# Kernel tuning notes

Hardware: AMD Instinct MI355X
Metric: run time of the kernel (lower is better)

Reference implementation:

```python
import jax, jax.numpy as jnp
import numpy as np

DEPTH = 256
SEQ = 394
EMB = 300


def _branch(x_nch, W, b, n):
    # W: [depth, n*EMB], flatten order of paragraph[i:i+n,:].flatten() is (time, emb)
    k = W.reshape(DEPTH, n, EMB).transpose(0, 2, 1)  # OIH: [depth, EMB, n]
    y = jax.lax.conv_general_dilated(
        x_nch, k, window_strides=(1,), padding='VALID',
        dimension_numbers=('NCH', 'OIH', 'NCH'))  # [B, depth, SEQ-n+1]
    # original loop only covers windows i = 0 .. SEQ-n-1 (SEQ-n windows)
    y = y[:, :, :SEQ - n] + b  # b: [depth, 1] broadcasts over time
    # running max starts at 0 and relu clamps >= 0; outer relu is a no-op
    return jnp.max(jax.nn.relu(y), axis=-1)  # [B, depth]


def setup_inputs() -> dict:
    key = jax.random.key(0)
    ks = jax.random.split(key, 7)
    inp = {
        'input': jax.random.normal(ks[0], (64, SEQ, EMB), dtype=jnp.float32),
        'W1': jax.random.normal(ks[1], (DEPTH, 3 * EMB), dtype=jnp.float32),
        'W2': jax.random.normal(ks[2], (DEPTH, 4 * EMB), dtype=jnp.float32),
        'W3': jax.random.normal(ks[3], (DEPTH, 5 * EMB), dtype=jnp.float32),
        'b1': jax.random.normal(ks[4], (DEPTH, 1), dtype=jnp.float32),
        'b2': jax.random.normal(ks[5], (DEPTH, 1), dtype=jnp.float32),
        'b3': jax.random.normal(ks[6], (DEPTH, 1), dtype=jnp.float32),
    }
    return inp


def reference(input, W1, W2, W3, b1, b2, b3):
    x = input.transpose(0, 2, 1)  # [B, EMB, SEQ] (NCH)
    o1 = _branch(x, W1, b1, 3)
    o2 = _branch(x, W2, b2, 4)
    o3 = _branch(x, W3, b3, 5)
    return jnp.concatenate([o1, o2, o3], axis=1)  # [B, 3*depth]
```

## Files before the change

kernel.cpp:

```cpp
#include <hip/hip_runtime.h>
#include <hip/hip_bf16.h>

#define SEQ 394
#define EMB 300
#define EMBP 312
#define NROWS (64 * SEQ)
#define XPTOT ((long)NROWS * EMBP)
#define NCHT 118
#define CBE0 29
#define CBE1 68
#define XE 36864
#define WGRAN ((long)NCHT * 1024)

typedef __attribute__((ext_vector_type(8))) short short8;
typedef __attribute__((ext_vector_type(4))) float f32x4;

__device__ __forceinline__ unsigned short f2b(float f) {
    unsigned u = __float_as_uint(f);
    u += 0x7FFFu + ((u >> 16) & 1u);
    return (unsigned short)(u >> 16);
}

__device__ __forceinline__ void gload_lds16(const void* g, void* l) {
    __builtin_amdgcn_global_load_lds(
        (const __attribute__((address_space(1))) void*)g,
        (__attribute__((address_space(3))) void*)l, 16, 0, 0);
}


__global__ __launch_bounds__(256)
void pack_x_kernel(const float* __restrict__ x, unsigned short* __restrict__ xp)
{
    long q = (long)blockIdx.x * 256 + threadIdx.x;
    int row = (int)(q / 78);
    int c4  = ((int)(q - (long)row * 78)) * 4;
    ushort4 u;
    if (c4 < 300) {
        float4 v = *(const float4*)(x + (long)row * 300 + c4);
        u = make_ushort4(f2b(v.x), f2b(v.y), f2b(v.z), f2b(v.w));
    } else {
        u = make_ushort4(0, 0, 0, 0);
    }
    *(ushort4*)(xp + q * 4) = u;
}

__global__ __launch_bounds__(256)
void pack_w_kernel(const float* __restrict__ W1, const float* __restrict__ W2,
                   const float* __restrict__ W3, unsigned short* __restrict__ wb)
{
    int G = blockIdx.x * 256 + threadIdx.x;
    int c    = G >> 10;
    int rem  = G & 1023;
    int fg   = rem >> 7;
    int floc = (rem >> 2) & 31;
    int gs   = rem & 3;
    const float* Wg; int n, cb;
    if (c <= CBE0)      { Wg = W1; n = 3; cb = 0;        }
    else if (c <= CBE1) { Wg = W2; n = 4; cb = CBE0 + 1; }
    else                { Wg = W3; n = 5; cb = CBE1 + 1; }
    const int K = n * 300;
    const int f = fg * 32 + floc;
    const int kl = (c - cb) * 32 + (gs ^ ((floc >> 1) & 3)) * 8;
    unsigned short v[8];
#pragma unroll
    for (int j = 0; j < 8; ++j) {
        int kk = kl + j;
        int r  = kk / EMBP;
        int e  = kk - r * EMBP;
        v[j] = (r < n && e < 300) ? f2b(Wg[(long)f * K + r * 300 + e]) : (unsigned short)0;
    }
    unsigned short* dst = wb + (long)G * 8;
    *(ushort4*)dst       = make_ushort4(v[0], v[1], v[2], v[3]);
    *(ushort4*)(dst + 4) = make_ushort4(v[4], v[5], v[6], v[7]);
}


__global__ __launch_bounds__(512, 2)
void convgemm_kernel(const unsigned short* __restrict__ xp,
                     const unsigned short* __restrict__ wb,
                     const float* __restrict__ b1, const float* __restrict__ b2,
                     const float* __restrict__ b3,
                     float* __restrict__ out)
{
    __shared__ unsigned short LDS[XE + 8 * 4096];

    const int tid  = threadIdx.x;
    const int lane = tid & 63;
    const int wid  = tid >> 6;
    const int lr   = lane & 15, lg = lane >> 4;
    const int b    = blockIdx.x >> 2;
    const int i0   = (blockIdx.x & 3) * 98;

    auto stageW = [&](int cc) {
        const unsigned short* ws = wb + ((long)(cc * 8 + wid)) * 1024 + lane * 8;
        unsigned short* wd = &LDS[XE + wid * 4096 + (cc & 3) * 1024];
        gload_lds16(ws, wd);
        gload_lds16(ws + 512, wd + 512);
    };

    {
        const long xbase = ((long)b * SEQ + i0) * EMBP;
        const long slim  = XPTOT - 8;
#pragma unroll
        for (int rd = 0; rd < 9; ++rd) {
            int g = rd * 512 + wid * 64;
            long se = xbase + (long)(g + lane) * 8;
            if (se > slim) se = slim;
            gload_lds16(xp + se, &LDS[g * 8]);
        }
    }
    stageW(0); stageW(1); stageW(2);
    asm volatile("s_waitcnt vmcnt(0)" ::: "memory");
    __builtin_amdgcn_sched_barrier(0);
    __builtin_amdgcn_s_barrier();
    __builtin_amdgcn_sched_barrier(0);

    f32x4 acc[2][7];
#pragma unroll
    for (int i = 0; i < 2; ++i)
#pragma unroll
        for (int j = 0; j < 7; ++j)
            acc[i][j] = (f32x4)0.0f;

    const int swz = (lg ^ ((lr >> 1) & 3)) * 8;

    auto readFrags = [&](int cc, short8 af[2], short8 bx[7]) {
        const int c0  = (cc <= CBE0) ? 0 : (cc <= CBE1) ? (CBE0 + 1) : (CBE1 + 1);
        const int bxe = (cc - c0) * 32;
        const unsigned short* Wc = &LDS[XE + wid * 4096 + (cc & 3) * 1024];
        af[0] = *(const short8*)&Wc[lr * 32 + swz];
        af[1] = *(const short8*)&Wc[(16 + lr) * 32 + swz];
#pragma unroll
        for (int ni = 0; ni < 7; ++ni)
            bx[ni] = *(const short8*)&LDS[(ni * 16 + lr) * EMBP + bxe + lg * 8];
    };

    auto doMFMA = [&](short8 af[2], short8 bx[7]) {
#pragma unroll
        for (int mi = 0; mi < 2; ++mi)
#pragma unroll
            for (int ni = 0; ni < 7; ++ni)
                acc[mi][ni] = __builtin_amdgcn_mfma_f32_16x16x32_bf16(af[mi], bx[ni], acc[mi][ni], 0, 0, 0);
    };

    auto epilogue = [&](int br) {
        const float* bg = (br == 0) ? b1 : (br == 1) ? b2 : b3;
        const int Nw = 391 - br;
        int wlim = Nw - i0; if (wlim > 112) wlim = 112;
        const int ob = b * 768 + br * 256;
#pragma unroll
        for (int mi = 0; mi < 2; ++mi) {
#pragma unroll
            for (int r = 0; r < 4; ++r) {
                const int d = wid * 32 + mi * 16 + lg * 4 + r;
                const float bv = bg[d];
                float m = 0.f;
#pragma unroll
                for (int ni = 0; ni < 7; ++ni) {
                    int w = ni * 16 + lr;
                    float v = fmaxf(acc[mi][ni][r] + bv, 0.f);
                    if (w >= wlim) v = 0.f;
                    m = fmaxf(m, v);
                }
#pragma unroll
                for (int off = 1; off < 16; off <<= 1)
                    m = fmaxf(m, __shfl_xor(m, off));
                if (lr == 0)
                    atomicMax((int*)(out + ob + d), __float_as_int(m));
            }
        }
#pragma unroll
        for (int i = 0; i < 2; ++i)
#pragma unroll
            for (int j = 0; j < 7; ++j)
                acc[i][j] = (f32x4)0.0f;
    };

    short8 fa0[2], fb0[7], fa1[2], fb1[7];
    readFrags(0, fa0, fb0);

    for (int c = 0; c < NCHT; c += 2) {
        if (c + 3 < NCHT) stageW(c + 3);
        if (c + 3 < NCHT)      asm volatile("s_waitcnt vmcnt(4)" ::: "memory");
        else if (c + 2 < NCHT) asm volatile("s_waitcnt vmcnt(2)" ::: "memory");
        else                   asm volatile("s_waitcnt vmcnt(0)" ::: "memory");
        __builtin_amdgcn_sched_barrier(0);
        readFrags(c + 1, fa1, fb1);
        doMFMA(fa0, fb0);
        if (c == CBE1) epilogue(1);

        const int cc = c + 1;
        if (cc + 3 < NCHT) stageW(cc + 3);
        if (cc + 3 < NCHT)      asm volatile("s_waitcnt vmcnt(4)" ::: "memory");
        else if (cc + 2 < NCHT) asm volatile("s_waitcnt vmcnt(2)" ::: "memory");
        else                    asm volatile("s_waitcnt vmcnt(0)" ::: "memory");
        __builtin_amdgcn_sched_barrier(0);
        if (cc + 1 < NCHT) readFrags(cc + 1, fa0, fb0);
        doMFMA(fa1, fb1);
        if (cc == CBE0) epilogue(0);
        if (cc == NCHT - 1) epilogue(2);
    }
}


__device__ __forceinline__ void load_chunk(const float* __restrict__ Wg,
                                           const float* __restrict__ xb,
                                           int K, int dbase, int i0, int k0, int tid,
                                           float4 wv[4], float4 xv[4])
{
#pragma unroll
    for (int i = 0; i < 4; ++i) {
        int fi  = tid + (i << 8);
        int row = fi >> 3;
        int c4  = (fi & 7) << 2;
        int col = k0 + c4;
        if (col < K)
            wv[i] = *(const float4*)(Wg + (long)(dbase + row) * K + col);
        else
            wv[i] = make_float4(0.f, 0.f, 0.f, 0.f);
        int off = (i0 + row) * EMB + col;
        int lim = SEQ * EMB - 4;
        if (off > lim) off = lim;
        xv[i] = *(const float4*)(xb + off);
    }
}

__device__ __forceinline__ void write_chunk(unsigned short (*Wb)[40],
                                            unsigned short (*Xb)[40],
                                            int tid, const float4 wv[4], const float4 xv[4])
{
#pragma unroll
    for (int i = 0; i < 4; ++i) {
        int fi  = tid + (i << 8);
        int row = fi >> 3;
        int c4  = (fi & 7) << 2;
        *(ushort4*)&Wb[row][c4] = make_ushort4(f2b(wv[i].x), f2b(wv[i].y), f2b(wv[i].z), f2b(wv[i].w));
        *(ushort4*)&Xb[row][c4] = make_ushort4(f2b(xv[i].x), f2b(xv[i].y), f2b(xv[i].z), f2b(xv[i].w));
    }
}

__global__ __launch_bounds__(256, 2)
void convmax_fallback(const float* __restrict__ x,
                      const float* __restrict__ W1, const float* __restrict__ W2,
                      const float* __restrict__ W3,
                      const float* __restrict__ b1, const float* __restrict__ b2,
                      const float* __restrict__ b3,
                      float* __restrict__ out)
{
    const int br = blockIdx.z;
    const int K  = (br == 0) ? 900 : (br == 1) ? 1200 : 1500;
    const int Nw = SEQ - 3 - br;
    const float* Wg = (br == 0) ? W1 : (br == 1) ? W2 : W3;
    const float* bg = (br == 0) ? b1 : (br == 1) ? b2 : b3;
    const int b  = blockIdx.x;
    const int mt = blockIdx.y >> 2;
    const int nt = blockIdx.y & 3;
    const int dbase = mt * 128;
    const int i0    = nt * 128;
    const float* xb = x + b * (SEQ * EMB);
    const int nch = (K + 31) >> 5;

    __shared__ unsigned short Wl[2][128][40];
    __shared__ unsigned short Xl[2][128][40];

    const int tid  = threadIdx.x;
    const int lane = tid & 63;
    const int wid  = tid >> 6;
    const int wr = wid >> 1, wc = wid & 1;
    const int lr = lane & 15, lg = lane >> 4;

    f32x4 acc[4][4];
#pragma unroll
    for (int i = 0; i < 4; ++i)
#pragma unroll
        for (int j = 0; j < 4; ++j)
            acc[i][j] = (f32x4)0.0f;

    {
        float4 wv[4], xv[4];
        load_chunk(Wg, xb, K, dbase, i0, 0, tid, wv, xv);
        write_chunk(Wl[0], Xl[0], tid, wv, xv);
    }
    __syncthreads();

    for (int c = 0; c < nch; ++c) {
        const int cur = c & 1;
        float4 wv[4], xv[4];
        const bool pf = (c + 1 < nch);
        if (pf) load_chunk(Wg, xb, K, dbase, i0, (c + 1) << 5, tid, wv, xv);

        short8 af[4], bfr[4];
#pragma unroll
        for (int mi = 0; mi < 4; ++mi)
            af[mi] = *(const short8*)&Wl[cur][wr * 64 + mi * 16 + lr][lg * 8];
#pragma unroll
        for (int ni = 0; ni < 4; ++ni)
            bfr[ni] = *(const short8*)&Xl[cur][wc * 64 + ni * 16 + lr][lg * 8];
#pragma unroll
        for (int mi = 0; mi < 4; ++mi)
#pragma unroll
            for (int ni = 0; ni < 4; ++ni)
                acc[mi][ni] = __builtin_amdgcn_mfma_f32_16x16x32_bf16(af[mi], bfr[ni], acc[mi][ni], 0, 0, 0);

        if (pf) write_chunk(Wl[cur ^ 1], Xl[cur ^ 1], tid, wv, xv);
        __syncthreads();
    }

    const int ob = b * 768 + br * 256;
#pragma unroll
    for (int mi = 0; mi < 4; ++mi) {
#pragma unroll
        for (int rI = 0; rI < 4; ++rI) {
            const int d = dbase + wr * 64 + mi * 16 + lg * 4 + rI;
            const float bv = bg[d];
            float m = 0.f;
#pragma unroll
            for (int ni = 0; ni < 4; ++ni) {
                int win = i0 + wc * 64 + ni * 16 + lr;
                float v = acc[mi][ni][rI] + bv;
                v = fmaxf(v, 0.f);
                if (win >= Nw) v = 0.f;
                m = fmaxf(m, v);
            }
#pragma unroll
            for (int off = 1; off < 16; off <<= 1)
                m = fmaxf(m, __shfl_xor(m, off));
            if (lr == 0)
                atomicMax((int*)(out + ob + d), __float_as_int(m));
        }
    }
}


extern "C" void kernel_launch(void* const* d_in, const int* in_sizes, int n_in,
                              void* d_out, int out_size, void* d_ws, size_t ws_size,
                              hipStream_t stream) {
    const float* x  = (const float*)d_in[0];
    const float* W1 = (const float*)d_in[1];
    const float* W2 = (const float*)d_in[2];
    const float* W3 = (const float*)d_in[3];
    const float* b1 = (const float*)d_in[4];
    const float* b2 = (const float*)d_in[5];
    const float* b3 = (const float*)d_in[6];
    float* out = (float*)d_out;

    hipMemsetAsync(d_out, 0, (size_t)out_size * sizeof(float), stream);

    const long WBTOT = WGRAN * 8;
    const size_t need = (size_t)(XPTOT + WBTOT) * 2;

    if (ws_size >= need) {
        unsigned short* xp = (unsigned short*)d_ws;
        unsigned short* wbb = xp + XPTOT;

        pack_x_kernel<<<7683, 256, 0, stream>>>(x, xp);
        pack_w_kernel<<<472, 256, 0, stream>>>(W1, W2, W3, wbb);
        convgemm_kernel<<<256, 512, 0, stream>>>(xp, wbb, b1, b2, b3, out);
    } else {
        dim3 grid(64, 8, 3);
        convmax_fallback<<<grid, 256, 0, stream>>>(x, W1, W2, W3, b1, b2, b3, out);
    }
}
```

Before: 88.22 us.

## Switch conv GEMM to 32x32 MFMA with register-direct weight loads

The main kernel moves from 16x16x32 to 32x32x16 bf16 MFMA tiles. Each wave now covers 64 filters by 64 windows instead of 32 filters by all 112 windows. Weights are loaded straight from global memory into registers in an MFMA-ready packed layout, replacing the swizzled LDS staging and explicit vmcnt waits, so LDS holds only the input tile. The window tiles are realigned with overlapping offsets so that 128 windows per block cover the sequence. This aims to cut LDS traffic and raise MFMA efficiency, at the cost of more global weight loads per wave and reliance on compiler scheduling to hide their latency.

```diff
diff --git a/kernel.cpp b/kernel.cpp
--- a/kernel.cpp
+++ b/kernel.cpp
@@ -9,11 +9,10 @@
 #define NCHT 118
 #define CBE0 29
 #define CBE1 68
-#define XE 36864
-#define WGRAN ((long)NCHT * 1024)
+#define XELEM 45056
 
 typedef __attribute__((ext_vector_type(8))) short short8;
-typedef __attribute__((ext_vector_type(4))) float f32x4;
+typedef __attribute__((ext_vector_type(16))) float f32x16;
 
 __device__ __forceinline__ unsigned short f2b(float f) {
     unsigned u = __float_as_uint(f);
@@ -49,18 +48,17 @@
                    const float* __restrict__ W3, unsigned short* __restrict__ wb)
 {
     int G = blockIdx.x * 256 + threadIdx.x;
-    int c    = G >> 10;
-    int rem  = G & 1023;
-    int fg   = rem >> 7;
-    int floc = (rem >> 2) & 31;
-    int gs   = rem & 3;
+    int l  = G & 63;
+    int ks = (G >> 6) & 1;
+    int g  = (G >> 7) & 7;
+    int c  = G >> 10;
     const float* Wg; int n, cb;
     if (c <= CBE0)      { Wg = W1; n = 3; cb = 0;        }
     else if (c <= CBE1) { Wg = W2; n = 4; cb = CBE0 + 1; }
     else                { Wg = W3; n = 5; cb = CBE1 + 1; }
     const int K = n * 300;
-    const int f = fg * 32 + floc;
-    const int kl = (c - cb) * 32 + (gs ^ ((floc >> 1) & 3)) * 8;
+    const int f = g * 32 + (l & 31);
+    const int kl = (c - cb) * 32 + ks * 16 + (l >> 5) * 8;
     unsigned short v[8];
 #pragma unroll
     for (int j = 0; j < 8; ++j) {
@@ -82,126 +80,126 @@
                      const float* __restrict__ b3,
                      float* __restrict__ out)
 {
-    __shared__ unsigned short LDS[XE + 8 * 4096];
+    __shared__ unsigned short X[XELEM];
 
     const int tid  = threadIdx.x;
     const int lane = tid & 63;
     const int wid  = tid >> 6;
-    const int lr   = lane & 15, lg = lane >> 4;
+    const int wfs  = wid >> 1;
+    const int ws   = wid & 1;
+    const int lm   = lane & 31;
+    const int l5   = lane >> 5;
     const int b    = blockIdx.x >> 2;
-    const int i0   = (blockIdx.x & 3) * 98;
-
-    auto stageW = [&](int cc) {
-        const unsigned short* ws = wb + ((long)(cc * 8 + wid)) * 1024 + lane * 8;
-        unsigned short* wd = &LDS[XE + wid * 4096 + (cc & 3) * 1024];
-        gload_lds16(ws, wd);
-        gload_lds16(ws + 512, wd + 512);
+    const int ti   = blockIdx.x & 3;
+    const int woff = (ti == 0) ? 0 : (ti == 1) ? 88 : (ti == 2) ? 176 : 263;
+
+    {
+        const long xbase = ((long)b * SEQ + woff) * EMBP;
+        const long slim  = XPTOT - 8;
+#pragma unroll
+        for (int rd = 0; rd < 11; ++rd) {
+            long se = xbase + (long)(rd * 512 + tid) * 8;
+            if (se > slim) se = slim;
+            gload_lds16(xp + se, &X[(rd * 512 + wid * 64) * 8]);
+        }
+    }
+    __syncthreads();
+
+    const unsigned short* wp0 = wb + ((long)(wfs * 2) * 128 + lane) * 8;
+    auto LDW = [&](int c, short8 w[2][2]) {
+        const short8* p = (const short8*)(wp0 + (long)c * 8192);
+        w[0][0] = p[0];   w[0][1] = p[64];
+        w[1][0] = p[128]; w[1][1] = p[192];
     };
 
-    {
-        const long xbase = ((long)b * SEQ + i0) * EMBP;
-        const long slim  = XPTOT - 8;
-#pragma unroll
-        for (int rd = 0; rd < 9; ++rd) {
-            int g = rd * 512 + wid * 64;
-            long se = xbase + (long)(g + lane) * 8;
-            if (se > slim) se = slim;
-            gload_lds16(xp + se, &LDS[g * 8]);
-        }
-    }
-    stageW(0); stageW(1); stageW(2);
-    asm volatile("s_waitcnt vmcnt(0)" ::: "memory");
-    __builtin_amdgcn_sched_barrier(0);
-    __builtin_amdgcn_s_barrier();
-    __builtin_amdgcn_sched_barrier(0);
-
-    f32x4 acc[2][7];
+    const unsigned short* xr0 = &X[(ws * 64 + lm) * EMBP + l5 * 8];
+    const unsigned short* xr1 = xr0 + 32 * EMBP;
+    auto RDBX = [&](int ko, short8 bx[2][2]) {
+        bx[0][0] = *(const short8*)(xr0 + ko);
+        bx[0][1] = *(const short8*)(xr0 + ko + 16);
+        bx[1][0] = *(const short8*)(xr1 + ko);
+        bx[1][1] = *(const short8*)(xr1 + ko + 16);
+    };
+
+    f32x16 acc[2][2];
 #pragma unroll
     for (int i = 0; i < 2; ++i)
 #pragma unroll
-        for (int j = 0; j < 7; ++j)
-            acc[i][j] = (f32x4)0.0f;
-
-    const int swz = (lg ^ ((lr >> 1) & 3)) * 8;
-
-    auto readFrags = [&](int cc, short8 af[2], short8 bx[7]) {
-        const int c0  = (cc <= CBE0) ? 0 : (cc <= CBE1) ? (CBE0 + 1) : (CBE1 + 1);
-        const int bxe = (cc - c0) * 32;
-        const unsigned short* Wc = &LDS[XE + wid * 4096 + (cc & 3) * 1024];
-        af[0] = *(const short8*)&Wc[lr * 32 + swz];
-        af[1] = *(const short8*)&Wc[(16 + lr) * 32 + swz];
-#pragma unroll
-        for (int ni = 0; ni < 7; ++ni)
-            bx[ni] = *(const short8*)&LDS[(ni * 16 + lr) * EMBP + bxe + lg * 8];
+        for (int j = 0; j < 2; ++j)
+            acc[i][j] = (f32x16)0.0f;
+
+    auto MFMA8 = [&](short8 w[2][2], short8 bx[2][2]) {
+#pragma unroll
+        for (int mi = 0; mi < 2; ++mi)
+#pragma unroll
+            for (int ni = 0; ni < 2; ++ni) {
+                acc[mi][ni] = __builtin_amdgcn_mfma_f32_32x32x16_bf16(w[mi][0], bx[ni][0], acc[mi][ni], 0, 0, 0);
+                acc[mi][ni] = __builtin_amdgcn_mfma_f32_32x32x16_bf16(w[mi][1], bx[ni][1], acc[mi][ni], 0, 0, 0);
+            }
     };
 
-    auto doMFMA = [&](short8 af[2], short8 bx[7]) {
-#pragma unroll
-        for (int mi = 0; mi < 2; ++mi)
-#pragma unroll
-            for (int ni = 0; ni < 7; ++ni)
-                acc[mi][ni] = __builtin_amdgcn_mfma_f32_16x16x32_bf16(af[mi], bx[ni], acc[mi][ni], 0, 0, 0);
-    };
-
-    auto epilogue = [&](int br) {
+    auto EPI = [&](int br) {
         const float* bg = (br == 0) ? b1 : (br == 1) ? b2 : b3;
         const int Nw = 391 - br;
-        int wlim = Nw - i0; if (wlim > 112) wlim = 112;
         const int ob = b * 768 + br * 256;
 #pragma unroll
         for (int mi = 0; mi < 2; ++mi) {
 #pragma unroll
-            for (int r = 0; r < 4; ++r) {
-                const int d = wid * 32 + mi * 16 + lg * 4 + r;
+            for (int r = 0; r < 16; ++r) {
+                const int d = wfs * 64 + mi * 32 + (r & 3) + 8 * (r >> 2) + 4 * l5;
                 const float bv = bg[d];
                 float m = 0.f;
 #pragma unroll
-                for (int ni = 0; ni < 7; ++ni) {
-                    int w = ni * 16 + lr;
+                for (int ni = 0; ni < 2; ++ni) {
+                    int w = woff + ws * 64 + ni * 32 + lm;
                     float v = fmaxf(acc[mi][ni][r] + bv, 0.f);
-                    if (w >= wlim) v = 0.f;
+                    if (w >= Nw) v = 0.f;
                     m = fmaxf(m, v);
                 }
 #pragma unroll
-                for (int off = 1; off < 16; off <<= 1)
+                for (int off = 1; off < 32; off <<= 1)
                     m = fmaxf(m, __shfl_xor(m, off));
-                if (lr == 0)
+                if (lm == 0)
                     atomicMax((int*)(out + ob + d), __float_as_int(m));
             }
         }
 #pragma unroll
         for (int i = 0; i < 2; ++i)
 #pragma unroll
-            for (int j = 0; j < 7; ++j)
-                acc[i][j] = (f32x4)0.0f;
+            for (int j = 0; j < 2; ++j)
+                acc[i][j] = (f32x16)0.0f;
     };
 
-    short8 fa0[2], fb0[7], fa1[2], fb1[7];
-    readFrags(0, fa0, fb0);
+    short8 wA[2][2], wB[2][2], bxA[2][2], bxB[2][2];
+    LDW(0, wA); LDW(1, wB);
+    RDBX(0, bxA);
 
     for (int c = 0; c < NCHT; c += 2) {
-        if (c + 3 < NCHT) stageW(c + 3);
-        if (c + 3 < NCHT)      asm volatile("s_waitcnt vmcnt(4)" ::: "memory");
-        else if (c + 2 < NCHT) asm volatile("s_waitcnt vmcnt(2)" ::: "memory");
-        else                   asm volatile("s_waitcnt vmcnt(0)" ::: "memory");
-        __builtin_amdgcn_sched_barrier(0);
-        readFrags(c + 1, fa1, fb1);
-        doMFMA(fa0, fb0);
-        if (c == CBE1) epilogue(1);
-
-        const int cc = c + 1;
-        if (cc + 3 < NCHT) stageW(cc + 3);
-        if (cc + 3 < NCHT)      asm volatile("s_waitcnt vmcnt(4)" ::: "memory");
-        else if (cc + 2 < NCHT) asm volatile("s_waitcnt vmcnt(2)" ::: "memory");
-        else                    asm volatile("s_waitcnt vmcnt(0)" ::: "memory");
-        __builtin_amdgcn_sched_barrier(0);
-        if (cc + 1 < NCHT) readFrags(cc + 1, fa0, fb0);
-        doMFMA(fa1, fb1);
-        if (cc == CBE0) epilogue(0);
-        if (cc == NCHT - 1) epilogue(2);
-    }
-}
-
+        {
+            const int t = c + 1;
+            const int ko = (t >= 69) ? (t - 69) * 32 : (t >= 30) ? (t - 30) * 32 : t * 32;
+            RDBX(ko, bxB);
+        }
+        MFMA8(wA, bxA);
+        if (c + 2 < NCHT) LDW(c + 2, wA);
+        if (c == CBE1) EPI(1);
+
+        {
+            const int t = c + 2;
+            if (t < NCHT) {
+                const int ko = (t >= 69) ? (t - 69) * 32 : (t >= 30) ? (t - 30) * 32 : t * 32;
+                RDBX(ko, bxA);
+            }
+        }
+        MFMA8(wB, bxB);
+        if (c + 3 < NCHT) LDW(c + 3, wB);
+        if (c + 1 == CBE0) EPI(0);
+        if (c + 1 == NCHT - 1) EPI(2);
+    }
+}
+
+
+typedef __attribute__((ext_vector_type(4))) float f32x4;
 
 __device__ __forceinline__ void load_chunk(const float* __restrict__ Wg,
                                            const float* __restrict__ xb,
@@ -239,6 +237,8 @@
     }
 }
 
+typedef __attribute__((ext_vector_type(8))) short short8f;
+
 __global__ __launch_bounds__(256, 2)
 void convmax_fallback(const float* __restrict__ x,
                       const float* __restrict__ W1, const float* __restrict__ W2,
@@ -289,13 +289,13 @@
         const bool pf = (c + 1 < nch);
         if (pf) load_chunk(Wg, xb, K, dbase, i0, (c + 1) << 5, tid, wv, xv);
 
-        short8 af[4], bfr[4];
+        short8f af[4], bfr[4];
 #pragma unroll
         for (int mi = 0; mi < 4; ++mi)
-            af[mi] = *(const short8*)&Wl[cur][wr * 64 + mi * 16 + lr][lg * 8];
+            af[mi] = *(const short8f*)&Wl[cur][wr * 64 + mi * 16 + lr][lg * 8];
 #pragma unroll
         for (int ni = 0; ni < 4; ++ni)
-            bfr[ni] = *(const short8*)&Xl[cur][wc * 64 + ni * 16 + lr][lg * 8];
+            bfr[ni] = *(const short8f*)&Xl[cur][wc * 64 + ni * 16 + lr][lg * 8];
 #pragma unroll
         for (int mi = 0; mi < 4; ++mi)
 #pragma unroll
@@ -346,7 +346,7 @@
 
     hipMemsetAsync(d_out, 0, (size_t)out_size * sizeof(float), stream);
 
-    const long WBTOT = WGRAN * 8;
+    const long WBTOT = (long)NCHT * 8192;
     const size_t need = (size_t)(XPTOT + WBTOT) * 2;
 
     if (ws_size >= need) {
```

After: 133.0 us. 1.51x slower.
